# Kernel optimization log

Measured on AMD Instinct MI355X. Metric: run time of the kernel, lower is better.

## Reference

```python
import jax, jax.numpy as jnp
import numpy as np

N_HEAD = 32
N_KV_HEAD = 8
ROPE_THETA = 500000.0


def rotate_half(x):
    d = x.shape[-1] // 2
    return jnp.concatenate((-x[..., d:], x[..., :d]), axis=-1)


def setup_inputs() -> dict:
    key = jax.random.key(0)
    ks = jax.random.split(key, 5)
    C = 2048
    B, T = 2, 2048
    s = 1.0 / np.sqrt(C)
    return {
        "x": jax.random.normal(ks[0], (B, T, C), dtype=jnp.float32),
        "Wq": jax.random.normal(ks[1], (C, C), dtype=jnp.float32) * s,
        "Wk": jax.random.normal(ks[2], (C, 512), dtype=jnp.float32) * s,
        "Wv": jax.random.normal(ks[3], (C, 512), dtype=jnp.float32) * s,
        "Wo": jax.random.normal(ks[4], (C, C), dtype=jnp.float32) * s,
    }


def reference(x, Wq, Wk, Wv, Wo):
    B, T, C = x.shape
    H, KV = N_HEAD, N_KV_HEAD
    D = C // H
    n_rep = H // KV

    q = (x @ Wq).reshape(B, T, H, D).transpose(0, 2, 1, 3)   # [B,H,T,D]
    k = (x @ Wk).reshape(B, T, KV, D).transpose(0, 2, 1, 3)  # [B,KV,T,D]
    v = (x @ Wv).reshape(B, T, KV, D).transpose(0, 2, 1, 3)  # [B,KV,T,D]

    # RoPE: cos/sin of shape [1,1,T,D], broadcast over batch and heads
    inv_freq = 1.0 / (ROPE_THETA ** (jnp.arange(0, D, 2, dtype=jnp.float32) / D))
    freqs = jnp.arange(T, dtype=jnp.float32)[:, None] * inv_freq[None, :]  # [T,D/2]
    emb = jnp.concatenate((freqs, freqs), axis=-1)  # [T,D]
    cos = jnp.cos(emb)[None, None].astype(x.dtype)
    sin = jnp.sin(emb)[None, None].astype(x.dtype)

    q = q * cos + rotate_half(q) * sin
    k = k * cos + rotate_half(k) * sin

    # repeat_kv (GQA expansion): [B,KV,T,D] -> [B,H,T,D]
    k = jnp.repeat(k, n_rep, axis=1)
    v = jnp.repeat(v, n_rep, axis=1)

    scale = 1.0 / jnp.sqrt(jnp.asarray(D, dtype=x.dtype))
    scores = jnp.einsum("bhqd,bhkd->bhqk", q, k) * scale  # [B,H,T,T]
    causal = jnp.tril(jnp.ones((T, T), dtype=bool))
    scores = jnp.where(causal[None, None], scores, jnp.finfo(scores.dtype).min)
    attn = jax.nn.softmax(scores, axis=-1)
    y = jnp.einsum("bhqk,bhkd->bhqd", attn, v)  # [B,H,T,D]
    y = y.transpose(0, 2, 1, 3).reshape(B, T, C)
    return y @ Wo
```

## Files before the change

### kernel.cpp

```cpp
#include <hip/hip_runtime.h>

using u16 = unsigned short;
using u32 = unsigned int;

typedef __attribute__((ext_vector_type(8))) __bf16 bf16x8;
typedef __attribute__((ext_vector_type(4))) float f32x4;
typedef __attribute__((ext_vector_type(16))) float f32x16;

#define DEVI __device__ __forceinline__

DEVI float bf2f(u16 u) {
  union { u32 i; float f; } v; v.i = ((u32)u) << 16; return v.f;
}
DEVI u16 f2bf(float f) {
  union { float f; u32 u; } v; v.f = f;
  u32 u = v.u;
  u32 r = (u + 0x7fffu + ((u >> 16) & 1u)) >> 16;
  return (u16)r;
}
DEVI u32 pkbf(float a, float b) {
  union { __bf16 h[2]; u32 u; } t;
  t.h[0] = (__bf16)a; t.h[1] = (__bf16)b;
  return t.u;
}

DEVI void gload16(const u16* g, u16* l) {
  __builtin_amdgcn_global_load_lds(
      (const __attribute__((address_space(1))) void*)g,
      (__attribute__((address_space(3))) void*)l, 16, 0, 0);
}

DEVI bf16x8 packP(const float* pp) {
  u32 a01 = pkbf(pp[0], pp[1]);
  u32 a23 = pkbf(pp[2], pp[3]);
  u32 a45 = pkbf(pp[4], pp[5]);
  u32 a67 = pkbf(pp[6], pp[7]);
  asm volatile("v_permlane32_swap_b32 %0, %1" : "+v"(a01), "+v"(a45));
  asm volatile("v_permlane32_swap_b32 %0, %1" : "+v"(a23), "+v"(a67));
  union { u32 w[4]; bf16x8 v; } pf;
  pf.w[0] = a01; pf.w[1] = a23; pf.w[2] = a45; pf.w[3] = a67;
  return pf.v;
}

__global__ __launch_bounds__(256) void cvt_bf16_f32(const float* __restrict__ in,
                                                    u16* __restrict__ out, int n8) {
  int i = blockIdx.x * 256 + threadIdx.x;
  if (i >= n8) return;
  const float4* fin = (const float4*)in;
  float4 a = fin[i * 2], b = fin[i * 2 + 1];
  u16 o[8] = {f2bf(a.x), f2bf(a.y), f2bf(a.z), f2bf(a.w),
              f2bf(b.x), f2bf(b.y), f2bf(b.z), f2bf(b.w)};
  ((uint4*)out)[i] = *(const uint4*)o;
}

DEVI void tcvt64_body(const float* in, u16* out, int R, int Cc, int c0, int r0, int t,
                      u16 (*tile)[72]) {
  {
    int row = t >> 2, part = t & 3;
    const float* src = in + (size_t)(r0 + row) * Cc + c0 + part * 16;
    float4 f0 = ((const float4*)src)[0];
    float4 f1 = ((const float4*)src)[1];
    float4 f2 = ((const float4*)src)[2];
    float4 f3 = ((const float4*)src)[3];
    u16 v[16] = {f2bf(f0.x), f2bf(f0.y), f2bf(f0.z), f2bf(f0.w),
                 f2bf(f1.x), f2bf(f1.y), f2bf(f1.z), f2bf(f1.w),
                 f2bf(f2.x), f2bf(f2.y), f2bf(f2.z), f2bf(f2.w),
                 f2bf(f3.x), f2bf(f3.y), f2bf(f3.z), f2bf(f3.w)};
    *(uint4*)&tile[row][part * 16]     = ((const uint4*)v)[0];
    *(uint4*)&tile[row][part * 16 + 8] = ((const uint4*)v)[1];
  }
  __syncthreads();
  {
    int c = t & 63, rq = t >> 6;
    u16 v[16];
#pragma unroll
    for (int i = 0; i < 16; i++) v[i] = tile[rq * 16 + i][c];
    u16* dst = out + (size_t)(c0 + c) * R + r0 + rq * 16;
    ((uint4*)dst)[0] = ((const uint4*)v)[0];
    ((uint4*)dst)[1] = ((const uint4*)v)[1];
  }
}

__global__ __launch_bounds__(256) void transpose_cvt64(const float* __restrict__ in,
                                                       u16* __restrict__ out,
                                                       int R, int Cc) {
  __shared__ u16 tile[64][72];
  tcvt64_body(in, out, R, Cc, blockIdx.x * 64, blockIdx.y * 64, threadIdx.x, tile);
}

__global__ __launch_bounds__(256) void transpose_wqkv(const float* __restrict__ Wq,
                                                      const float* __restrict__ Wk,
                                                      const float* __restrict__ Wv,
                                                      u16* __restrict__ out) {
  __shared__ u16 tile[64][72];
  int bx = blockIdx.x;
  const float* in;
  u16* dst;
  int Cc, c0;
  if (bx < 32)      { in = Wq; dst = out;                        Cc = 2048; c0 = bx * 64; }
  else if (bx < 40) { in = Wk; dst = out + (size_t)2048 * 2048;  Cc = 512;  c0 = (bx - 32) * 64; }
  else              { in = Wv; dst = out + (size_t)2560 * 2048;  Cc = 512;  c0 = (bx - 40) * 64; }
  tcvt64_body(in, dst, 2048, Cc, c0, blockIdx.y * 64, threadIdx.x, tile);
}

__global__ __launch_bounds__(256) void transpose_sl64(const u16* __restrict__ in, int ldin,
                                                      u16* __restrict__ out,
                                                      int R, int Cc) {
  __shared__ u16 tile[64][72];
  int c0 = blockIdx.x * 64, r0 = blockIdx.y * 64;
  int t = threadIdx.x;
  {
    int row = t >> 2, part = t & 3;
    const u16* src = in + (size_t)(r0 + row) * ldin + c0 + part * 16;
    uint4 a = ((const uint4*)src)[0];
    uint4 b = ((const uint4*)src)[1];
    *(uint4*)&tile[row][part * 16]     = a;
    *(uint4*)&tile[row][part * 16 + 8] = b;
  }
  __syncthreads();
  {
    int c = t & 63, rq = t >> 6;
    u16 v[16];
#pragma unroll
    for (int i = 0; i < 16; i++) v[i] = tile[rq * 16 + i][c];
    u16* dst = out + (size_t)(c0 + c) * R + r0 + rq * 16;
    ((uint4*)dst)[0] = ((const uint4*)v)[0];
    ((uint4*)dst)[1] = ((const uint4*)v)[1];
  }
}

DEVI void cstore(u16* C, size_t idx, float v)   { C[idx] = f2bf(v); }
DEVI void cstore(float* C, size_t idx, float v) { C[idx] = v; }

template <typename TO, bool ROPE>
__global__ __launch_bounds__(256) void gemm128(const u16* __restrict__ A,
                                               const u16* __restrict__ Bt,
                                               TO* __restrict__ C,
                                               int M, int N, int K) {
  __shared__ u16 As[2 * 128 * 32];
  __shared__ u16 Bs[2 * 128 * 32];
  int tid = threadIdx.x, wid = tid >> 6, lane = tid & 63;
  int quad = lane >> 4, l15 = lane & 15;

  int nwg = gridDim.x * gridDim.y;
  int bid = blockIdx.y * gridDim.x + blockIdx.x;
  int swz = (bid & 7) * (nwg >> 3) + (bid >> 3);
  int bx = swz % gridDim.x, by = swz / gridDim.x;
  int m0 = by * 128, n0 = bx * 128;
  int wm = (wid >> 1) * 64, wn = (wid & 1) * 64;

  int r0s = wid * 16 + (lane >> 2);
  int r1s = 64 + wid * 16 + (lane >> 2);
  int cblk = lane & 3;
  int cs0 = (cblk ^ ((r0s >> 1) & 3)) * 8;
  int cs1 = (cblk ^ ((r1s >> 1) & 3)) * 8;
  u16* lA0 = As + wid * 512 + lane * 8;
  u16* lA1 = As + (4 + wid) * 512 + lane * 8;
  u16* lB0 = Bs + wid * 512 + lane * 8;
  u16* lB1 = Bs + (4 + wid) * 512 + lane * 8;
  const u16* gA0 = A + (size_t)(m0 + r0s) * K + cs0;
  const u16* gA1 = A + (size_t)(m0 + r1s) * K + cs1;
  const u16* gB0 = Bt + (size_t)(n0 + r0s) * K + cs0;
  const u16* gB1 = Bt + (size_t)(n0 + r1s) * K + cs1;

  f32x4 acc[4][4];
  for (int i = 0; i < 4; i++)
    for (int j = 0; j < 4; j++) acc[i][j] = f32x4{0.f, 0.f, 0.f, 0.f};

  gload16(gA0, lA0);
  gload16(gA1, lA1);
  gload16(gB0, lB0);
  gload16(gB1, lB1);
  __builtin_amdgcn_s_waitcnt(0x0F70);
  __syncthreads();

  int cur = 0;
  for (int k0 = 0; k0 < K; k0 += 32) {
    int nb = cur ^ 1;
    if (k0 + 32 < K) {
      gload16(gA0 + k0 + 32, lA0 + nb * 4096);
      gload16(gA1 + k0 + 32, lA1 + nb * 4096);
      gload16(gB0 + k0 + 32, lB0 + nb * 4096);
      gload16(gB1 + k0 + 32, lB1 + nb * 4096);
    }
    const u16* Ab = As + cur * 4096;
    const u16* Bb = Bs + cur * 4096;
    bf16x8 af[4], bf_[4];
    for (int mi = 0; mi < 4; mi++) {
      int row = wm + mi * 16 + l15;
      af[mi] = *(const bf16x8*)(Ab + row * 32 + ((quad ^ ((row >> 1) & 3)) * 8));
    }
    for (int ni = 0; ni < 4; ni++) {
      int row = wn + ni * 16 + l15;
      bf_[ni] = *(const bf16x8*)(Bb + row * 32 + ((quad ^ ((row >> 1) & 3)) * 8));
    }
    for (int mi = 0; mi < 4; mi++)
      for (int ni = 0; ni < 4; ni++)
        acc[mi][ni] = __builtin_amdgcn_mfma_f32_16x16x32_bf16(af[mi], bf_[ni], acc[mi][ni], 0, 0, 0);
    __builtin_amdgcn_s_waitcnt(0x0F70);
    __syncthreads();
    cur = nb;
  }

  if (ROPE) {
#pragma unroll
    for (int ni = 0; ni < 2; ni++) {
      int nc = n0 + wn + ni * 16;
      if (nc < 2560) {
        float scale = (nc < 2048) ? 0.18033688f : 1.0f;
        float inv = exp2f(-(float)(ni * 16 + l15) * 0.59161152f);
#pragma unroll
        for (int mi = 0; mi < 4; mi++)
#pragma unroll
          for (int r = 0; r < 4; r++) {
            int t = (m0 + wm + mi * 16 + quad * 4 + r) & 2047;
            float sn, cs;
            __sincosf((float)t * inv, &sn, &cs);
            float xl = acc[mi][ni][r], xh = acc[mi][ni + 2][r];
            acc[mi][ni][r]     = (xl * cs - xh * sn) * scale;
            acc[mi][ni + 2][r] = (xh * cs + xl * sn) * scale;
          }
      }
    }
  }

  for (int mi = 0; mi < 4; mi++)
    for (int ni = 0; ni < 4; ni++)
      for (int r = 0; r < 4; r++) {
        int row = m0 + wm + mi * 16 + quad * 4 + r;
        int col = n0 + wn + ni * 16 + l15;
        cstore(C, (size_t)row * N + col, acc[mi][ni][r]);
      }
}

__global__ __launch_bounds__(256) void attn64(const u16* __restrict__ QKV,
                                              const u16* __restrict__ Vt,
                                              u16* __restrict__ Y) {
  __shared__ u16 Ks[2 * 64 * 64];
  __shared__ u16 Vst[2 * 64 * 64];

  int tid = threadIdx.x, wid = tid >> 6, lane = tid & 63;
  int l31 = lane & 31, hi = lane >> 5;
  int bh = blockIdx.y, b = bh >> 5, h = bh & 31, kvh = h >> 2;
  int p = blockIdx.x;
  int jA = p, jB = 15 - p;

  int kr  = wid * 8 + (lane >> 3);
  int kgn = lane & 7;
  const u16* gK0 = QKV + (size_t)(b * 2048 + kr) * 3072 + 2048 + kvh * 64
                 + ((kgn ^ (kr & 7)) * 8);
  u16* lK0 = Ks + wid * 512 + lane * 8;

  int vr = tid >> 3, vg = tid & 7;
  const u16* gV0 = Vt + (size_t)(kvh * 64 + vr) * 4096 + b * 2048 + vg * 8;
  u16* lV0 = Vst + vr * 64 + ((vg ^ (vr & 7)) * 8);

  int q0wA = jA * 128 + wid * 32, qgA = q0wA + l31;
  int q0wB = jB * 128 + wid * 32, qgB = q0wB + l31;

  bf16x8 qfA[4], qfB[4];
  {
    const u16* qpA = QKV + (size_t)(b * 2048 + qgA) * 3072 + h * 64 + hi * 8;
    const u16* qpB = QKV + (size_t)(b * 2048 + qgB) * 3072 + h * 64 + hi * 8;
#pragma unroll
    for (int dh = 0; dh < 4; dh++) {
      qfA[dh] = *(const bf16x8*)(qpA + dh * 16);
      qfB[dh] = *(const bf16x8*)(qpB + dh * 16);
    }
  }

  f32x16 o0A, o1A, o0B, o1B;
#pragma unroll
  for (int i = 0; i < 16; i++) { o0A[i] = 0.f; o1A[i] = 0.f; o0B[i] = 0.f; o1B[i] = 0.f; }
  float zsumA = 0.f, zsumB = 0.f;

  int nkt = 2 * (jB + 1);

  {
    uint4 va = *(const uint4*)(gV0);
    uint4 vb = *(const uint4*)(gV0 + 32 * 4096);
    gload16(gK0, lK0);
    gload16(gK0 + 32 * 3072, lK0 + 2048);
    __builtin_amdgcn_s_waitcnt(0x0F70);
    *(uint4*)(lV0)        = va;
    *(uint4*)(lV0 + 2048) = vb;
  }
  __syncthreads();

  int cur = 0;
  for (int kt = 0; kt < nkt; kt++) {
    int kbase = kt * 64;
    int nxt = cur ^ 1;
    bool more = (kt + 1 < nkt);
    uint4 va, vb;
    if (more) {
      size_t ko = (size_t)(kbase + 64);
      va = *(const uint4*)(gV0 + ko);
      vb = *(const uint4*)(gV0 + 32 * 4096 + ko);
      gload16(gK0 + ko * 3072, lK0 + nxt * 4096);
      gload16(gK0 + ko * 3072 + 32 * 3072, lK0 + nxt * 4096 + 2048);
    }

    const u16* Kb = Ks + cur * 4096;
    const u16* Vb = Vst + cur * 4096;
#pragma unroll
    for (int sub = 0; sub < 2; sub++) {
      int kb = kbase + sub * 32;
      if (kb > q0wB) break;
      if (kb <= q0wA) {
        f32x16 sA, sB;
#pragma unroll
        for (int i = 0; i < 16; i++) { sA[i] = 0.f; sB[i] = 0.f; }
#pragma unroll
        for (int dh = 0; dh < 4; dh++) {
          int g = (dh * 2 + hi) ^ (l31 & 7);
          bf16x8 kf = *(const bf16x8*)(Kb + (sub * 32 + l31) * 64 + g * 8);
          sA = __builtin_amdgcn_mfma_f32_32x32x16_bf16(kf, qfA[dh], sA, 0, 0, 0);
          sB = __builtin_amdgcn_mfma_f32_32x32x16_bf16(kf, qfB[dh], sB, 0, 0, 0);
        }
        float pbA[16], pbB[16];
        if (kb < q0wA) {
#pragma unroll
          for (int r = 0; r < 16; r++) {
            float pv = exp2f(sA[r]);
            zsumA += pv;
            pbA[r] = pv;
          }
        } else {
#pragma unroll
          for (int r = 0; r < 16; r++) {
            int key = kb + (r & 3) + 8 * (r >> 2) + 4 * hi;
            float pv = (key <= qgA) ? exp2f(sA[r]) : 0.f;
            zsumA += pv;
            pbA[r] = pv;
          }
        }
#pragma unroll
        for (int r = 0; r < 16; r++) {
          float pv = exp2f(sB[r]);
          zsumB += pv;
          pbB[r] = pv;
        }
        bf16x8 pfA0 = packP(pbA), pfA1 = packP(pbA + 8);
        bf16x8 pfB0 = packP(pbB), pfB1 = packP(pbB + 8);
#pragma unroll
        for (int kk = 0; kk < 2; kk++) {
          int kgr = sub * 4 + kk * 2 + hi;
          const u16* vp = Vb + l31 * 64 + ((kgr ^ (l31 & 7)) * 8);
          bf16x8 v0 = *(const bf16x8*)(vp);
          bf16x8 v1 = *(const bf16x8*)(vp + 2048);
          bf16x8 pA = kk ? pfA1 : pfA0;
          bf16x8 pB = kk ? pfB1 : pfB0;
          o0A = __builtin_amdgcn_mfma_f32_32x32x16_bf16(pA, v0, o0A, 0, 0, 0);
          o1A = __builtin_amdgcn_mfma_f32_32x32x16_bf16(pA, v1, o1A, 0, 0, 0);
          o0B = __builtin_amdgcn_mfma_f32_32x32x16_bf16(pB, v0, o0B, 0, 0, 0);
          o1B = __builtin_amdgcn_mfma_f32_32x32x16_bf16(pB, v1, o1B, 0, 0, 0);
        }
      } else {
        f32x16 s;
#pragma unroll
        for (int i = 0; i < 16; i++) s[i] = 0.f;
#pragma unroll
        for (int dh = 0; dh < 4; dh++) {
          int g = (dh * 2 + hi) ^ (l31 & 7);
          bf16x8 kf = *(const bf16x8*)(Kb + (sub * 32 + l31) * 64 + g * 8);
          s = __builtin_amdgcn_mfma_f32_32x32x16_bf16(kf, qfB[dh], s, 0, 0, 0);
        }
        float pb[16];
        if (kb < q0wB) {
#pragma unroll
          for (int r = 0; r < 16; r++) {
            float pv = exp2f(s[r]);
            zsumB += pv;
            pb[r] = pv;
          }
        } else {
#pragma unroll
          for (int r = 0; r < 16; r++) {
            int key = kb + (r & 3) + 8 * (r >> 2) + 4 * hi;
            float pv = (key <= qgB) ? exp2f(s[r]) : 0.f;
            zsumB += pv;
            pb[r] = pv;
          }
        }
        bf16x8 pf0 = packP(pb), pf1 = packP(pb + 8);
#pragma unroll
        for (int kk = 0; kk < 2; kk++) {
          int kgr = sub * 4 + kk * 2 + hi;
          const u16* vp = Vb + l31 * 64 + ((kgr ^ (l31 & 7)) * 8);
          bf16x8 v0 = *(const bf16x8*)(vp);
          bf16x8 v1 = *(const bf16x8*)(vp + 2048);
          bf16x8 pB = kk ? pf1 : pf0;
          o0B = __builtin_amdgcn_mfma_f32_32x32x16_bf16(pB, v0, o0B, 0, 0, 0);
          o1B = __builtin_amdgcn_mfma_f32_32x32x16_bf16(pB, v1, o1B, 0, 0, 0);
        }
      }
    }

    if (more) {
      __builtin_amdgcn_s_waitcnt(0x0F70);
      *(uint4*)(lV0 + nxt * 4096)        = va;
      *(uint4*)(lV0 + nxt * 4096 + 2048) = vb;
    }
    __syncthreads();
    cur = nxt;
  }

  {
    float zf = zsumA + __shfl_xor(zsumA, 32);
#pragma unroll
    for (int r = 0; r < 16; r++) {
      int qr = (r & 3) + 8 * (r >> 2) + 4 * hi;
      float zr = __shfl(zf, qr, 64);
      float inv = 1.f / zr;
      size_t row = (size_t)(b * 2048 + q0wA + qr);
      Y[row * 2048 + h * 64 + l31]      = f2bf(o0A[r] * inv);
      Y[row * 2048 + h * 64 + 32 + l31] = f2bf(o1A[r] * inv);
    }
  }
  {
    float zf = zsumB + __shfl_xor(zsumB, 32);
#pragma unroll
    for (int r = 0; r < 16; r++) {
      int qr = (r & 3) + 8 * (r >> 2) + 4 * hi;
      float zr = __shfl(zf, qr, 64);
      float inv = 1.f / zr;
      size_t row = (size_t)(b * 2048 + q0wB + qr);
      Y[row * 2048 + h * 64 + l31]      = f2bf(o0B[r] * inv);
      Y[row * 2048 + h * 64 + 32 + l31] = f2bf(o1B[r] * inv);
    }
  }
}

extern "C" void kernel_launch(void* const* d_in, const int* in_sizes, int n_in,
                              void* d_out, int out_size, void* d_ws, size_t ws_size,
                              hipStream_t stream) {
  const float* x  = (const float*)d_in[0];
  const float* Wq = (const float*)d_in[1];
  const float* Wk = (const float*)d_in[2];
  const float* Wv = (const float*)d_in[3];
  const float* Wo = (const float*)d_in[4];
  float* outp = (float*)d_out;

  u16* xb    = (u16*)d_ws;
  u16* WqkvT = xb + 8388608;
  u16* QKV   = WqkvT + 6291456;
  u16* Vt    = QKV + 12582912;
  u16* Yb    = xb;
  u16* WoT   = WqkvT;

  cvt_bf16_f32<<<4096, 256, 0, stream>>>(x, xb, 1048576);

  transpose_wqkv<<<dim3(48, 32), 256, 0, stream>>>(Wq, Wk, Wv, WqkvT);

  gemm128<u16, true><<<dim3(24, 32), 256, 0, stream>>>(xb, WqkvT, QKV, 4096, 3072, 2048);

  transpose_sl64<<<dim3(8, 64), 256, 0, stream>>>(QKV + 2560, 3072, Vt, 4096, 512);

  attn64<<<dim3(8, 64), 256, 0, stream>>>(QKV, Vt, Yb);

  transpose_cvt64<<<dim3(32, 32), 256, 0, stream>>>(Wo, WoT, 2048, 2048);
  gemm128<float, false><<<dim3(16, 32), 256, 0, stream>>>(Yb, WoT, outp, 4096, 2048, 2048);
}
```

Baseline: 309.3 us.

## Fuse weight/input prep kernels and add MFMA priority hints in attention

When the workspace is large enough, one prep_all kernel now converts x to bf16 and transposes Wq/Wk/Wv and Wo, replacing three launches. WoT gets its own region so the Wo transpose no longer has to wait until after attention. Inside the attention loop, the MFMA sections are wrapped in s_setprio raises, and the row-sum accumulation becomes a tree reduction (sum16) after the exp loop instead of a serial add chain. The aim is to cut launch overhead, shorten dependency chains and help overlap MFMA with exp work across waves, at the cost of a workspace-size dependent code path.

```diff
diff --git a/kernel.cpp b/kernel.cpp
--- a/kernel.cpp
+++ b/kernel.cpp
@@ -42,15 +42,13 @@
   return pf.v;
 }
 
-__global__ __launch_bounds__(256) void cvt_bf16_f32(const float* __restrict__ in,
-                                                    u16* __restrict__ out, int n8) {
-  int i = blockIdx.x * 256 + threadIdx.x;
-  if (i >= n8) return;
-  const float4* fin = (const float4*)in;
-  float4 a = fin[i * 2], b = fin[i * 2 + 1];
-  u16 o[8] = {f2bf(a.x), f2bf(a.y), f2bf(a.z), f2bf(a.w),
-              f2bf(b.x), f2bf(b.y), f2bf(b.z), f2bf(b.w)};
-  ((uint4*)out)[i] = *(const uint4*)o;
+DEVI float sum16(const float* p) {
+  float a0 = p[0] + p[1],  a1 = p[2] + p[3];
+  float a2 = p[4] + p[5],  a3 = p[6] + p[7];
+  float a4 = p[8] + p[9],  a5 = p[10] + p[11];
+  float a6 = p[12] + p[13], a7 = p[14] + p[15];
+  float b0 = a0 + a1, b1 = a2 + a3, b2 = a4 + a5, b3 = a6 + a7;
+  return (b0 + b1) + (b2 + b3);
 }
 
 DEVI void tcvt64_body(const float* in, u16* out, int R, int Cc, int c0, int r0, int t,
@@ -79,6 +77,17 @@
     ((uint4*)dst)[0] = ((const uint4*)v)[0];
     ((uint4*)dst)[1] = ((const uint4*)v)[1];
   }
+}
+
+__global__ __launch_bounds__(256) void cvt_bf16_f32(const float* __restrict__ in,
+                                                    u16* __restrict__ out, int n8) {
+  int i = blockIdx.x * 256 + threadIdx.x;
+  if (i >= n8) return;
+  const float4* fin = (const float4*)in;
+  float4 a = fin[i * 2], b = fin[i * 2 + 1];
+  u16 o[8] = {f2bf(a.x), f2bf(a.y), f2bf(a.z), f2bf(a.w),
+              f2bf(b.x), f2bf(b.y), f2bf(b.z), f2bf(b.w)};
+  ((uint4*)out)[i] = *(const uint4*)o;
 }
 
 __global__ __launch_bounds__(256) void transpose_cvt64(const float* __restrict__ in,
@@ -103,6 +112,42 @@
   tcvt64_body(in, dst, 2048, Cc, c0, blockIdx.y * 64, threadIdx.x, tile);
 }
 
+__global__ __launch_bounds__(256) void prep_all(const float* __restrict__ x,
+                                                const float* __restrict__ Wq,
+                                                const float* __restrict__ Wk,
+                                                const float* __restrict__ Wv,
+                                                const float* __restrict__ Wo,
+                                                u16* __restrict__ xb,
+                                                u16* __restrict__ WqkvT,
+                                                u16* __restrict__ WoT) {
+  __shared__ u16 tile[64][72];
+  int id = blockIdx.x;
+  if (id < 4096) {
+    int i = id * 256 + threadIdx.x;
+    const float4* fin = (const float4*)x;
+    float4 a = fin[i * 2], b = fin[i * 2 + 1];
+    u16 o[8] = {f2bf(a.x), f2bf(a.y), f2bf(a.z), f2bf(a.w),
+                f2bf(b.x), f2bf(b.y), f2bf(b.z), f2bf(b.w)};
+    ((uint4*)xb)[i] = *(const uint4*)o;
+    return;
+  }
+  id -= 4096;
+  if (id < 1536) {
+    int bx = id % 48, by = id / 48;
+    const float* in;
+    u16* dst;
+    int Cc, c0;
+    if (bx < 32)      { in = Wq; dst = WqkvT;                        Cc = 2048; c0 = bx * 64; }
+    else if (bx < 40) { in = Wk; dst = WqkvT + (size_t)2048 * 2048;  Cc = 512;  c0 = (bx - 32) * 64; }
+    else              { in = Wv; dst = WqkvT + (size_t)2560 * 2048;  Cc = 512;  c0 = (bx - 40) * 64; }
+    tcvt64_body(in, dst, 2048, Cc, c0, by * 64, threadIdx.x, tile);
+    return;
+  }
+  id -= 1536;
+  int bx = id & 31, by = id >> 5;
+  tcvt64_body(Wo, WoT, 2048, 2048, bx * 64, by * 64, threadIdx.x, tile);
+}
+
 __global__ __launch_bounds__(256) void transpose_sl64(const u16* __restrict__ in, int ldin,
                                                       u16* __restrict__ out,
                                                       int R, int Cc) {
@@ -311,6 +356,7 @@
         f32x16 sA, sB;
 #pragma unroll
         for (int i = 0; i < 16; i++) { sA[i] = 0.f; sB[i] = 0.f; }
+        __builtin_amdgcn_s_setprio(1);
 #pragma unroll
         for (int dh = 0; dh < 4; dh++) {
           int g = (dh * 2 + hi) ^ (l31 & 7);
@@ -318,31 +364,25 @@
           sA = __builtin_amdgcn_mfma_f32_32x32x16_bf16(kf, qfA[dh], sA, 0, 0, 0);
           sB = __builtin_amdgcn_mfma_f32_32x32x16_bf16(kf, qfB[dh], sB, 0, 0, 0);
         }
+        __builtin_amdgcn_s_setprio(0);
         float pbA[16], pbB[16];
         if (kb < q0wA) {
 #pragma unroll
-          for (int r = 0; r < 16; r++) {
-            float pv = exp2f(sA[r]);
-            zsumA += pv;
-            pbA[r] = pv;
-          }
+          for (int r = 0; r < 16; r++) pbA[r] = exp2f(sA[r]);
         } else {
 #pragma unroll
           for (int r = 0; r < 16; r++) {
             int key = kb + (r & 3) + 8 * (r >> 2) + 4 * hi;
-            float pv = (key <= qgA) ? exp2f(sA[r]) : 0.f;
-            zsumA += pv;
-            pbA[r] = pv;
+            pbA[r] = (key <= qgA) ? exp2f(sA[r]) : 0.f;
           }
         }
 #pragma unroll
-        for (int r = 0; r < 16; r++) {
-          float pv = exp2f(sB[r]);
-          zsumB += pv;
-          pbB[r] = pv;
-        }
+        for (int r = 0; r < 16; r++) pbB[r] = exp2f(sB[r]);
+        zsumA += sum16(pbA);
+        zsumB += sum16(pbB);
         bf16x8 pfA0 = packP(pbA), pfA1 = packP(pbA + 8);
         bf16x8 pfB0 = packP(pbB), pfB1 = packP(pbB + 8);
+        __builtin_amdgcn_s_setprio(1);
 #pragma unroll
         for (int kk = 0; kk < 2; kk++) {
           int kgr = sub * 4 + kk * 2 + hi;
@@ -356,34 +396,33 @@
           o0B = __builtin_amdgcn_mfma_f32_32x32x16_bf16(pB, v0, o0B, 0, 0, 0);
           o1B = __builtin_amdgcn_mfma_f32_32x32x16_bf16(pB, v1, o1B, 0, 0, 0);
         }
+        __builtin_amdgcn_s_setprio(0);
       } else {
         f32x16 s;
 #pragma unroll
         for (int i = 0; i < 16; i++) s[i] = 0.f;
+        __builtin_amdgcn_s_setprio(1);
 #pragma unroll
         for (int dh = 0; dh < 4; dh++) {
           int g = (dh * 2 + hi) ^ (l31 & 7);
           bf16x8 kf = *(const bf16x8*)(Kb + (sub * 32 + l31) * 64 + g * 8);
           s = __builtin_amdgcn_mfma_f32_32x32x16_bf16(kf, qfB[dh], s, 0, 0, 0);
         }
+        __builtin_amdgcn_s_setprio(0);
         float pb[16];
         if (kb < q0wB) {
 #pragma unroll
-          for (int r = 0; r < 16; r++) {
-            float pv = exp2f(s[r]);
-            zsumB += pv;
-            pb[r] = pv;
-          }
+          for (int r = 0; r < 16; r++) pb[r] = exp2f(s[r]);
         } else {
 #pragma unroll
           for (int r = 0; r < 16; r++) {
             int key = kb + (r & 3) + 8 * (r >> 2) + 4 * hi;
-            float pv = (key <= qgB) ? exp2f(s[r]) : 0.f;
-            zsumB += pv;
-            pb[r] = pv;
+            pb[r] = (key <= qgB) ? exp2f(s[r]) : 0.f;
           }
         }
+        zsumB += sum16(pb);
         bf16x8 pf0 = packP(pb), pf1 = packP(pb + 8);
+        __builtin_amdgcn_s_setprio(1);
 #pragma unroll
         for (int kk = 0; kk < 2; kk++) {
           int kgr = sub * 4 + kk * 2 + hi;
@@ -394,6 +433,7 @@
           o0B = __builtin_amdgcn_mfma_f32_32x32x16_bf16(pB, v0, o0B, 0, 0, 0);
           o1B = __builtin_amdgcn_mfma_f32_32x32x16_bf16(pB, v1, o1B, 0, 0, 0);
         }
+        __builtin_amdgcn_s_setprio(0);
       }
     }
 
@@ -447,11 +487,16 @@
   u16* QKV   = WqkvT + 6291456;
   u16* Vt    = QKV + 12582912;
   u16* Yb    = xb;
-  u16* WoT   = WqkvT;
-
-  cvt_bf16_f32<<<4096, 256, 0, stream>>>(x, xb, 1048576);
-
-  transpose_wqkv<<<dim3(48, 32), 256, 0, stream>>>(Wq, Wk, Wv, WqkvT);
+
+  bool bigws = ws_size >= (size_t)(33554432) * 2;
+  u16* WoT = bigws ? (Vt + 2097152) : WqkvT;
+
+  if (bigws) {
+    prep_all<<<6656, 256, 0, stream>>>(x, Wq, Wk, Wv, Wo, xb, WqkvT, WoT);
+  } else {
+    cvt_bf16_f32<<<4096, 256, 0, stream>>>(x, xb, 1048576);
+    transpose_wqkv<<<dim3(48, 32), 256, 0, stream>>>(Wq, Wk, Wv, WqkvT);
+  }
 
   gemm128<u16, true><<<dim3(24, 32), 256, 0, stream>>>(xb, WqkvT, QKV, 4096, 3072, 2048);
 
@@ -459,6 +504,8 @@
 
   attn64<<<dim3(8, 64), 256, 0, stream>>>(QKV, Vt, Yb);
 
-  transpose_cvt64<<<dim3(32, 32), 256, 0, stream>>>(Wo, WoT, 2048, 2048);
+  if (!bigws) {
+    transpose_cvt64<<<dim3(32, 32), 256, 0, stream>>>(Wo, WoT, 2048, 2048);
+  }
   gemm128<float, false><<<dim3(16, 32), 256, 0, stream>>>(Yb, WoT, outp, 4096, 2048, 2048);
 }
```

After: 308.3 us, median of 3. Within noise of the previous version (-0.3%).
